# Performance work log

Measured on AMD Instinct MI355X. Metric: run time of the kernel, lower is better.

Reference implementation:

```python
import jax, jax.numpy as jnp
import numpy as np

N, E = 40000, 640000
IN_DIM, EDGE_DIM, HID, H1 = 5, 11, 128, 4
NEG_SLOPE = 0.2


def _add_self_loops(ei, ea, n):
    # PyG GATConv default: add_self_loops=True, fill_value='mean' for edge_attr
    loop = jnp.arange(n, dtype=ei.dtype)
    ei2 = jnp.concatenate([ei, jnp.stack([loop, loop])], axis=1)
    ea2 = jnp.concatenate([ea, jnp.broadcast_to(ea.mean(0), (n, ea.shape[1]))], axis=0)
    return ei2, ea2


def _gat(x, ei, ea, W, We, a_src, a_dst, a_edge, b, H, C):
    # Single GATConv layer (eval mode, dropout inactive)
    n = x.shape[0]
    xh = (x @ W).reshape(n, H, C)            # [N,H,C]
    eh = (ea @ We).reshape(-1, H, C)         # [E,H,C]
    src, dst = ei[0], ei[1]
    a_s = (xh * a_src).sum(-1)               # [N,H]
    a_d = (xh * a_dst).sum(-1)               # [N,H]
    alpha = jax.nn.leaky_relu(a_s[src] + a_d[dst] + (eh * a_edge).sum(-1), NEG_SLOPE)  # [E,H]
    amax = jax.ops.segment_max(alpha, dst, num_segments=n)
    ex = jnp.exp(alpha - amax[dst])
    den = jax.ops.segment_sum(ex, dst, num_segments=n)
    w = ex / (den[dst] + 1e-16)              # softmax over inbound edges per dst
    out = jax.ops.segment_sum(xh[src] * w[:, :, None], dst, num_segments=n)  # [N,H,C]
    return out.reshape(n, H * C) + b


def setup_inputs() -> dict:
    key = jax.random.key(0)
    ks = jax.random.split(key, 20)
    s = 0.1
    return {
        "x": jax.random.normal(ks[0], (N, IN_DIM), jnp.float32),
        "edge_index": jax.random.randint(ks[1], (2, E), 0, N),
        "edge_attr": jax.random.normal(ks[2], (E, EDGE_DIM), jnp.float32),
        "W1": jax.random.normal(ks[3], (IN_DIM, H1 * HID), jnp.float32) * s,
        "We1": jax.random.normal(ks[4], (EDGE_DIM, H1 * HID), jnp.float32) * s,
        "a_src1": jax.random.normal(ks[5], (H1, HID), jnp.float32) * s,
        "a_dst1": jax.random.normal(ks[6], (H1, HID), jnp.float32) * s,
        "a_edge1": jax.random.normal(ks[7], (H1, HID), jnp.float32) * s,
        "b1": jnp.zeros((H1 * HID,), jnp.float32),
        # layer 2 (512 -> 128, 1 head)
        "W2": jax.random.normal(ks[8], (H1 * HID, HID), jnp.float32) * s,
        "We2": jax.random.normal(ks[9], (EDGE_DIM, HID), jnp.float32) * s,
        "a_src2": jax.random.normal(ks[10], (1, HID), jnp.float32) * s,
        "a_dst2": jax.random.normal(ks[11], (1, HID), jnp.float32) * s,
        "a_edge2": jax.random.normal(ks[12], (1, HID), jnp.float32) * s,
        "b2": jnp.zeros((HID,), jnp.float32),
        # final linear 128 -> 1
        "Wfc": jax.random.normal(ks[13], (HID, 1), jnp.float32) * s,
        "bfc": jnp.zeros((1,), jnp.float32),
    }


def reference(x, edge_index, edge_attr,
              W1, We1, a_src1, a_dst1, a_edge1, b1,
              W2, We2, a_src2, a_dst2, a_edge2, b2,
              Wfc, bfc):
    ei, ea = _add_self_loops(edge_index, edge_attr, x.shape[0])
    h = jax.nn.relu(_gat(x, ei, ea, W1, We1, a_src1, a_dst1, a_edge1, b1, H1, HID))
    h = jax.nn.relu(_gat(h, ei, ea, W2, We2, a_src2, a_dst2, a_edge2, b2, 1, HID))
    return jax.nn.sigmoid(h @ Wfc + bfc)
```

## Files before the change

kernel.cpp:

```cpp
#include <hip/hip_runtime.h>

#define NN   40000
#define EE   640000
#define IND  5
#define ED   11
#define HIDD 128
#define F1   512
#define EB   1250

typedef unsigned short u16;
typedef unsigned int   u32;
typedef __attribute__((ext_vector_type(8))) short bf16x8;
typedef __attribute__((ext_vector_type(4))) float f32x4;

__device__ __forceinline__ float bf2f(u16 u) { return __uint_as_float(((u32)u) << 16); }
__device__ __forceinline__ u16 f2bf(float f) {
    u32 u = __float_as_uint(f);
    return (u16)((u + 0x7FFFu + ((u >> 16) & 1u)) >> 16);
}

__device__ __forceinline__ float wsum(float v) {
#pragma unroll
    for (int o = 32; o; o >>= 1) v += __shfl_xor(v, o, 64);
    return v;
}
__device__ __forceinline__ float lrelu(float v) { return v > 0.f ? v : 0.2f * v; }


#define SBLK 256
#define SGRID ((NN + SBLK - 1) / SBLK)
#define PREPG (EB + 33)

__global__ void __launch_bounds__(256) k_prep(const int* __restrict__ ei,
                                              int* __restrict__ counts,
                                              int* __restrict__ rank,
                                              float* __restrict__ consts,
                                              const float* __restrict__ ea,
                                              float* __restrict__ psum,
                                              const float* __restrict__ We1,
                                              const float* __restrict__ ae1,
                                              const float* __restrict__ We2,
                                              const float* __restrict__ ae2,
                                              const float* __restrict__ W2,
                                              u16* __restrict__ bsw,
                                              const float* __restrict__ W1,
                                              const float* __restrict__ as1,
                                              const float* __restrict__ ad1) {
    __shared__ float shf[4 * ED];
    int bid = blockIdx.x, t = threadIdx.x;
    if (bid < EB) {
        int i0 = bid * 512 + t;
        int i1 = i0 + 256;
        int d0 = ei[EE + i0];
        int d1 = ei[EE + i1];
        int rk0 = atomicAdd(&counts[d0], 1);
        int rk1 = atomicAdd(&counts[d1], 1);
        rank[i0] = rk0;
        rank[i1] = rk1;
        const float* r0 = ea + (size_t)i0 * ED;
        const float* r1 = ea + (size_t)i1 * ED;
        float r[ED];
#pragma unroll
        for (int k = 0; k < ED; ++k) r[k] = r0[k] + r1[k];
#pragma unroll
        for (int k = 0; k < ED; ++k) r[k] = wsum(r[k]);
        int wv = t >> 6, lane = t & 63;
#pragma unroll
        for (int k = 0; k < ED; ++k)
            if (lane == k) shf[wv * ED + k] = r[k];
        __syncthreads();
        if (t < ED)
            psum[(size_t)bid * ED + t] =
                shf[t] + shf[ED + t] + shf[2 * ED + t] + shf[3 * ED + t];
        return;
    }
    if (bid == EB) {
        if (t < 44) {
            int k = t >> 2, h = t & 3;
            float s = 0.f;
            for (int c = 0; c < HIDD; ++c)
                s += We1[k * F1 + h * HIDD + c] * ae1[h * HIDD + c];
            consts[16 + t] = s;
        }
        if (t >= 48 && t < 48 + ED) {
            int k = t - 48;
            float s = 0.f;
            for (int c = 0; c < HIDD; ++c)
                s += We2[k * HIDD + c] * ae2[c];
            consts[64 + k] = s;
        }
        if (t >= 64 && t < 84) {
            int idx = t - 64, j = idx >> 2, h = idx & 3;
            float s = 0.f;
            for (int c = 0; c < HIDD; ++c)
                s += W1[j * F1 + h * HIDD + c] * as1[h * HIDD + c];
            consts[100 + idx] = s;
        }
        if (t >= 84 && t < 104) {
            int idx = t - 84, j = idx >> 2, h = idx & 3;
            float s = 0.f;
            for (int c = 0; c < HIDD; ++c)
                s += W1[j * F1 + h * HIDD + c] * ad1[h * HIDD + c];
            consts[120 + idx] = s;
        }
        return;
    }
    int t2 = (bid - (EB + 1)) * 256 + t;
    if (t2 >= 8192) return;
    int lane = t2 & 63, ks = (t2 >> 6) & 15, nt = t2 >> 10;
    int kbase = ks * 32 + (lane >> 4) * 8;
    int n = nt * 16 + (lane & 15);
    size_t dst = (size_t)t2 * 8;
#pragma unroll
    for (int j = 0; j < 8; ++j)
        bsw[dst + j] = f2bf(W2[(size_t)(kbase + j) * HIDD + n]);
}

__global__ void __launch_bounds__(SBLK) k_scan(const int* __restrict__ counts,
                                               int* __restrict__ row_off,
                                               const float* __restrict__ x,
                                               float* __restrict__ consts,
                                               float* __restrict__ aS1,
                                               float* __restrict__ aD1,
                                               const float* __restrict__ psum) {
    __shared__ int shi[SBLK];
    __shared__ float shf[4 * ED];
    __shared__ float mean[ED];
    __shared__ int s_boff;
    int t = threadIdx.x, b = blockIdx.x;
    if (b < SGRID) {
        int acc = 0;
        for (int i = t; i < b * SBLK; i += SBLK) acc += counts[i];
        shi[t] = acc;
        __syncthreads();
        for (int o = 128; o; o >>= 1) {
            if (t < o) shi[t] += shi[t + o];
            __syncthreads();
        }
        if (t == 0) s_boff = shi[0];
        __syncthreads();
        int boff = s_boff;
        __syncthreads();
        int i = b * SBLK + t;
        int v = (i < NN) ? counts[i] : 0;
        shi[t] = v;
        __syncthreads();
        for (int o = 1; o < SBLK; o <<= 1) {
            int u = (t >= o) ? shi[t - o] : 0;
            __syncthreads();
            shi[t] += u;
            __syncthreads();
        }
        if (i < NN) row_off[i] = boff + shi[t] - v;
        if (b == 0 && t == 0) row_off[NN] = EE;
        return;
    }
    if (b == SGRID * 2) {
        float acc[ED];
#pragma unroll
        for (int k = 0; k < ED; ++k) acc[k] = 0.f;
        for (int w = t; w < EB; w += SBLK) {
            const float* p = psum + (size_t)w * ED;
#pragma unroll
            for (int k = 0; k < ED; ++k) acc[k] += p[k];
        }
#pragma unroll
        for (int k = 0; k < ED; ++k) acc[k] = wsum(acc[k]);
        int wv = t >> 6, lane = t & 63;
#pragma unroll
        for (int k = 0; k < ED; ++k)
            if (lane == k) shf[wv * ED + k] = acc[k];
        __syncthreads();
        if (t < ED)
            mean[t] = (shf[t] + shf[ED + t] + shf[2 * ED + t] + shf[3 * ED + t])
                      * (1.0f / (float)EE);
        __syncthreads();
        if (t < 4) {
            float s = 0.f;
            for (int k = 0; k < ED; ++k) s += mean[k] * consts[16 + k * 4 + t];
            consts[80 + t] = s;
        }
        if (t == 8) {
            float s = 0.f;
            for (int k = 0; k < ED; ++k) s += mean[k] * consts[64 + k];
            consts[96] = s;
        }
        return;
    }
    int n = (b - SGRID) * SBLK + t;
    if (n >= NN) return;
    const float* xp = x + (size_t)n * IND;
    float xv0 = xp[0], xv1 = xp[1], xv2 = xp[2], xv3 = xp[3], xv4 = xp[4];
    float4 s4, d4;
    float* sp = (float*)&s4;
    float* dp = (float*)&d4;
#pragma unroll
    for (int h = 0; h < 4; ++h) {
        sp[h] = xv0 * consts[100 + 0 * 4 + h] + xv1 * consts[100 + 1 * 4 + h]
              + xv2 * consts[100 + 2 * 4 + h] + xv3 * consts[100 + 3 * 4 + h]
              + xv4 * consts[100 + 4 * 4 + h];
        dp[h] = xv0 * consts[120 + 0 * 4 + h] + xv1 * consts[120 + 1 * 4 + h]
              + xv2 * consts[120 + 2 * 4 + h] + xv3 * consts[120 + 3 * 4 + h]
              + xv4 * consts[120 + 4 * 4 + h];
    }
    *(float4*)(aS1 + (size_t)n * 4) = s4;
    *(float4*)(aD1 + (size_t)n * 4) = d4;
}

__global__ void __launch_bounds__(256) k_build(const float* __restrict__ ea,
                                               const int* __restrict__ ei,
                                               const int* __restrict__ rank,
                                               const int* __restrict__ row_off,
                                               const float* __restrict__ consts,
                                               uint4* __restrict__ rec) {
    int t = threadIdx.x;
    int i0 = blockIdx.x * 512 + t;
    int i1 = i0 + 256;
    int s0v = ei[i0], s1v = ei[i1];
    int d0 = ei[EE + i0], d1 = ei[EE + i1];
    int p0 = row_off[d0] + rank[i0];
    int p1 = row_off[d1] + rank[i1];
    const float* r0 = ea + (size_t)i0 * ED;
    const float* r1 = ea + (size_t)i1 * ED;
    float a0 = 0.f, a1 = 0.f, a2 = 0.f, a3 = 0.f, a4 = 0.f;
    float b0 = 0.f, b1 = 0.f, b2 = 0.f, b3 = 0.f, b4 = 0.f;
#pragma unroll
    for (int k = 0; k < ED; ++k) {
        float c0 = consts[16 + k * 4 + 0], c1 = consts[16 + k * 4 + 1];
        float c2 = consts[16 + k * 4 + 2], c3 = consts[16 + k * 4 + 3];
        float ct = consts[64 + k];
        float v0 = r0[k], v1 = r1[k];
        a0 += v0 * c0; a1 += v0 * c1; a2 += v0 * c2; a3 += v0 * c3; a4 += v0 * ct;
        b0 += v1 * c0; b1 += v1 * c1; b2 += v1 * c2; b3 += v1 * c3; b4 += v1 * ct;
    }
    uint4 q0, q1;
    q0.x = (u32)f2bf(a0) | ((u32)f2bf(a1) << 16);
    q0.y = (u32)f2bf(a2) | ((u32)f2bf(a3) << 16);
    q0.z = (u32)s0v;
    q0.w = __float_as_uint(a4);
    q1.x = (u32)f2bf(b0) | ((u32)f2bf(b1) << 16);
    q1.y = (u32)f2bf(b2) | ((u32)f2bf(b3) << 16);
    q1.z = (u32)s1v;
    q1.w = __float_as_uint(b4);
    rec[p0] = q0;
    rec[p1] = q1;
}

__global__ void __launch_bounds__(256) k_agg1g(const int* __restrict__ row_off,
                                               const uint4* __restrict__ rec,
                                               const float* __restrict__ aS1,
                                               const float* __restrict__ aD1,
                                               const float* __restrict__ x,
                                               const float* __restrict__ W1,
                                               const float* __restrict__ b1,
                                               const float* __restrict__ consts,
                                               const u16* __restrict__ bsw,
                                               const float* __restrict__ as2,
                                               const float* __restrict__ ad2,
                                               u16* __restrict__ xh2,
                                               float* __restrict__ aS2,
                                               float* __restrict__ aD2) {
    __shared__ u16 hA[16 * 512];
    __shared__ float sh_ps[4][16], sh_pd[4][16];
    int wv = threadIdx.x >> 6, lane = threadIdx.x & 63;
    int g = lane >> 4, sl = lane & 15;
    int row = wv * 4 + g;
    int n0 = blockIdx.x * 16;
    int n = n0 + row;
    int s0 = row_off[n], s1 = row_off[n + 1];
    float4 adv = *(const float4*)(aD1 + (size_t)n * 4);
    float z0 = 0.f, z1 = 0.f, z2 = 0.f, z3 = 0.f;
    float xa[4][5];
#pragma unroll
    for (int h = 0; h < 4; ++h)
#pragma unroll
        for (int j = 0; j < 5; ++j) xa[h][j] = 0.f;

    for (int i = s0 + sl; i < s1; i += 16) {
        uint4 q = rec[i];
        int s = (int)q.z;
        float e0 = bf2f((u16)(q.x & 0xFFFF)), e1 = bf2f((u16)(q.x >> 16));
        float e2 = bf2f((u16)(q.y & 0xFFFF)), e3 = bf2f((u16)(q.y >> 16));
        float4 as4 = *(const float4*)(aS1 + (size_t)s * 4);
        const float* xp = x + (size_t)s * IND;
        float x0 = xp[0], x1 = xp[1], x2 = xp[2], x3 = xp[3], x4 = xp[4];
        float ex;
        ex = __expf(lrelu(e0 + as4.x + adv.x)); z0 += ex;
        xa[0][0] += ex * x0; xa[0][1] += ex * x1; xa[0][2] += ex * x2;
        xa[0][3] += ex * x3; xa[0][4] += ex * x4;
        ex = __expf(lrelu(e1 + as4.y + adv.y)); z1 += ex;
        xa[1][0] += ex * x0; xa[1][1] += ex * x1; xa[1][2] += ex * x2;
        xa[1][3] += ex * x3; xa[1][4] += ex * x4;
        ex = __expf(lrelu(e2 + as4.z + adv.z)); z2 += ex;
        xa[2][0] += ex * x0; xa[2][1] += ex * x1; xa[2][2] += ex * x2;
        xa[2][3] += ex * x3; xa[2][4] += ex * x4;
        ex = __expf(lrelu(e3 + as4.w + adv.w)); z3 += ex;
        xa[3][0] += ex * x0; xa[3][1] += ex * x1; xa[3][2] += ex * x2;
        xa[3][3] += ex * x3; xa[3][4] += ex * x4;
    }
    if (sl == 0) {
        float4 as4 = *(const float4*)(aS1 + (size_t)n * 4);
        const float* xp = x + (size_t)n * IND;
        float x0 = xp[0], x1 = xp[1], x2 = xp[2], x3 = xp[3], x4 = xp[4];
        float ex;
        ex = __expf(lrelu(consts[80] + as4.x + adv.x)); z0 += ex;
        xa[0][0] += ex * x0; xa[0][1] += ex * x1; xa[0][2] += ex * x2;
        xa[0][3] += ex * x3; xa[0][4] += ex * x4;
        ex = __expf(lrelu(consts[81] + as4.y + adv.y)); z1 += ex;
        xa[1][0] += ex * x0; xa[1][1] += ex * x1; xa[1][2] += ex * x2;
        xa[1][3] += ex * x3; xa[1][4] += ex * x4;
        ex = __expf(lrelu(consts[82] + as4.z + adv.z)); z2 += ex;
        xa[2][0] += ex * x0; xa[2][1] += ex * x1; xa[2][2] += ex * x2;
        xa[2][3] += ex * x3; xa[2][4] += ex * x4;
        ex = __expf(lrelu(consts[83] + as4.w + adv.w)); z3 += ex;
        xa[3][0] += ex * x0; xa[3][1] += ex * x1; xa[3][2] += ex * x2;
        xa[3][3] += ex * x3; xa[3][4] += ex * x4;
    }
#pragma unroll
    for (int o = 1; o <= 8; o <<= 1) {
        z0 += __shfl_xor(z0, o, 64); z1 += __shfl_xor(z1, o, 64);
        z2 += __shfl_xor(z2, o, 64); z3 += __shfl_xor(z3, o, 64);
#pragma unroll
        for (int h = 0; h < 4; ++h)
#pragma unroll
            for (int j = 0; j < 5; ++j) xa[h][j] += __shfl_xor(xa[h][j], o, 64);
    }
    float zz[4] = {z0, z1, z2, z3};
#pragma unroll
    for (int cb = 0; cb < 4; ++cb) {
        float ih = 1.f / (zz[cb] + 1e-16f);
        int c0 = cb * 128 + sl * 8;
        u32 wp[4];
#pragma unroll
        for (int jj = 0; jj < 4; ++jj) {
            int c = c0 + jj * 2;
            float v0 = (xa[cb][0] * W1[0 * F1 + c] + xa[cb][1] * W1[1 * F1 + c]
                      + xa[cb][2] * W1[2 * F1 + c] + xa[cb][3] * W1[3 * F1 + c]
                      + xa[cb][4] * W1[4 * F1 + c]) * ih;
            float v1 = (xa[cb][0] * W1[0 * F1 + c + 1] + xa[cb][1] * W1[1 * F1 + c + 1]
                      + xa[cb][2] * W1[2 * F1 + c + 1] + xa[cb][3] * W1[3 * F1 + c + 1]
                      + xa[cb][4] * W1[4 * F1 + c + 1]) * ih;
            v0 = fmaxf(v0 + b1[c], 0.f);
            v1 = fmaxf(v1 + b1[c + 1], 0.f);
            wp[jj] = (u32)f2bf(v0) | ((u32)f2bf(v1) << 16);
        }
        uint4 st; st.x = wp[0]; st.y = wp[1]; st.z = wp[2]; st.w = wp[3];
        int cbyte = (cb * 256 + sl * 16) ^ ((row & 7) << 4);
        *(uint4*)((char*)hA + row * 1024 + cbyte) = st;
    }
    __syncthreads();

    int mrow = lane & 15, quad = lane >> 4;
    const u16* bbase = bsw + lane * 8;
    int nt0 = wv * 2;
    f32x4 acc0 = (f32x4){0.f, 0.f, 0.f, 0.f};
    f32x4 acc1 = (f32x4){0.f, 0.f, 0.f, 0.f};
    const char* arow = (const char*)hA + mrow * 1024;
    int axor = (mrow & 7) << 4;
    bf16x8 af0 = *(const bf16x8*)(arow + ((quad * 16 + 0) ^ axor));
    bf16x8 af1;
    bf16x8 b00 = *(const bf16x8*)(bbase + (size_t)nt0 * 8192);
    bf16x8 b01 = *(const bf16x8*)(bbase + (size_t)(nt0 + 1) * 8192);
    bf16x8 n00, n01;
#pragma unroll
    for (int ks = 0; ks < 16; ++ks) {
        if (ks < 15) {
            af1 = *(const bf16x8*)(arow + ((quad * 16 + (ks + 1) * 64) ^ axor));
            n00 = *(const bf16x8*)(bbase + (size_t)nt0 * 8192 + (ks + 1) * 512);
            n01 = *(const bf16x8*)(bbase + (size_t)(nt0 + 1) * 8192 + (ks + 1) * 512);
        }
        acc0 = __builtin_amdgcn_mfma_f32_16x16x32_bf16(af0, b00, acc0, 0, 0, 0);
        acc1 = __builtin_amdgcn_mfma_f32_16x16x32_bf16(af0, b01, acc1, 0, 0, 0);
        af0 = af1; b00 = n00; b01 = n01;
    }
    float ps[4] = {0.f, 0.f, 0.f, 0.f}, pd[4] = {0.f, 0.f, 0.f, 0.f};
    {
        int col = nt0 * 16 + mrow;
        float sa = as2[col], da = ad2[col];
#pragma unroll
        for (int r = 0; r < 4; ++r) {
            float v = acc0[r];
            xh2[(size_t)(n0 + quad * 4 + r) * HIDD + col] = f2bf(v);
            ps[r] += v * sa; pd[r] += v * da;
        }
    }
    {
        int col = (nt0 + 1) * 16 + mrow;
        float sa = as2[col], da = ad2[col];
#pragma unroll
        for (int r = 0; r < 4; ++r) {
            float v = acc1[r];
            xh2[(size_t)(n0 + quad * 4 + r) * HIDD + col] = f2bf(v);
            ps[r] += v * sa; pd[r] += v * da;
        }
    }
#pragma unroll
    for (int r = 0; r < 4; ++r) {
#pragma unroll
        for (int o = 1; o <= 8; o <<= 1) {
            ps[r] += __shfl_xor(ps[r], o, 64);
            pd[r] += __shfl_xor(pd[r], o, 64);
        }
        if (mrow == 0) {
            sh_ps[wv][quad * 4 + r] = ps[r];
            sh_pd[wv][quad * 4 + r] = pd[r];
        }
    }
    __syncthreads();
    int t = threadIdx.x;
    if (t < 16) {
        float s = sh_ps[0][t] + sh_ps[1][t] + sh_ps[2][t] + sh_ps[3][t];
        aS2[n0 + t] = s;
    } else if (t < 32) {
        int r = t - 16;
        float s = sh_pd[0][r] + sh_pd[1][r] + sh_pd[2][r] + sh_pd[3][r];
        aD2[n0 + r] = s;
    }
}

__global__ void __launch_bounds__(256) k_agg2(const int* __restrict__ row_off,
                                              const uint4* __restrict__ rec,
                                              const float* __restrict__ aS2,
                                              const float* __restrict__ aD2,
                                              const u16* __restrict__ xh2,
                                              const float* __restrict__ bias2,
                                              const float* __restrict__ Wfc,
                                              const float* __restrict__ bfc,
                                              const float* __restrict__ consts,
                                              float* __restrict__ out) {
    int n = blockIdx.x * 4 + (threadIdx.x >> 6);
    int t = threadIdx.x & 63;
    int s0 = row_off[n], s1 = row_off[n + 1];
    float adn = aD2[n];
    int g = t >> 4, l = t & 15;
    int c0 = l * 8;
    float z = 0.f;
    float acc[8];
#pragma unroll
    for (int j = 0; j < 8; ++j) acc[j] = 0.f;
    for (int i = s0 + g; i < s1; i += 4) {
        uint4 qe = rec[i];
        int s = (int)qe.z;
        float et2 = __uint_as_float(qe.w);
        float ex = __expf(lrelu(aS2[s] + adn + et2));
        z += ex;
        uint4 q = *(const uint4*)(xh2 + (size_t)s * HIDD + c0);
        acc[0] += ex * bf2f((u16)(q.x & 0xFFFF)); acc[1] += ex * bf2f((u16)(q.x >> 16));
        acc[2] += ex * bf2f((u16)(q.y & 0xFFFF)); acc[3] += ex * bf2f((u16)(q.y >> 16));
        acc[4] += ex * bf2f((u16)(q.z & 0xFFFF)); acc[5] += ex * bf2f((u16)(q.z >> 16));
        acc[6] += ex * bf2f((u16)(q.w & 0xFFFF)); acc[7] += ex * bf2f((u16)(q.w >> 16));
    }
    if (g == 0) {
        float ex = __expf(lrelu(aS2[n] + adn + consts[96]));
        z += ex;
        uint4 q = *(const uint4*)(xh2 + (size_t)n * HIDD + c0);
        acc[0] += ex * bf2f((u16)(q.x & 0xFFFF)); acc[1] += ex * bf2f((u16)(q.x >> 16));
        acc[2] += ex * bf2f((u16)(q.y & 0xFFFF)); acc[3] += ex * bf2f((u16)(q.y >> 16));
        acc[4] += ex * bf2f((u16)(q.z & 0xFFFF)); acc[5] += ex * bf2f((u16)(q.z >> 16));
        acc[6] += ex * bf2f((u16)(q.w & 0xFFFF)); acc[7] += ex * bf2f((u16)(q.w >> 16));
    }
#pragma unroll
    for (int o = 16; o <= 32; o <<= 1) {
        z += __shfl_xor(z, o, 64);
#pragma unroll
        for (int j = 0; j < 8; ++j) acc[j] += __shfl_xor(acc[j], o, 64);
    }
    float inv = 1.f / (z + 1e-16f);
    float p = 0.f;
#pragma unroll
    for (int j = 0; j < 8; ++j) {
        float o = fmaxf(acc[j] * inv + bias2[c0 + j], 0.f);
        p += o * Wfc[c0 + j];
    }
#pragma unroll
    for (int o = 1; o <= 8; o <<= 1) p += __shfl_xor(p, o, 64);
    if (t == 0) {
        float logit = p + bfc[0];
        out[n] = 1.f / (1.f + __expf(-logit));
    }
}

extern "C" void kernel_launch(void* const* d_in, const int* in_sizes, int n_in,
                              void* d_out, int out_size, void* d_ws, size_t ws_size,
                              hipStream_t stream) {
    (void)in_sizes; (void)n_in; (void)out_size; (void)ws_size;
    const float* x   = (const float*)d_in[0];
    const int*   ei  = (const int*)d_in[1];
    const float* ea  = (const float*)d_in[2];
    const float* W1  = (const float*)d_in[3];
    const float* We1 = (const float*)d_in[4];
    const float* as1 = (const float*)d_in[5];
    const float* ad1 = (const float*)d_in[6];
    const float* ae1 = (const float*)d_in[7];
    const float* b1  = (const float*)d_in[8];
    const float* W2  = (const float*)d_in[9];
    const float* We2 = (const float*)d_in[10];
    const float* as2 = (const float*)d_in[11];
    const float* ad2 = (const float*)d_in[12];
    const float* ae2 = (const float*)d_in[13];
    const float* b2v = (const float*)d_in[14];
    const float* Wfc = (const float*)d_in[15];
    const float* bfc = (const float*)d_in[16];
    float* out = (float*)d_out;

    char* ws = (char*)d_ws;
    size_t off = 0;
    auto take = [&](size_t nb) {
        size_t r = off;
        off += (nb + 255) & ~(size_t)255;
        return r;
    };
    float* consts = (float*)(ws + take(1024));
    int*   counts = (int*)(ws + take((size_t)NN * 4));
    size_t zbytes = off;
    int* row_off  = (int*)(ws + take((size_t)(NN + 1) * 4));
    int* rank     = (int*)(ws + take((size_t)EE * 4));
    float* psum   = (float*)(ws + take((size_t)EB * ED * 4));
    uint4* rec    = (uint4*)(ws + take((size_t)EE * 16));
    float* aS1    = (float*)(ws + take((size_t)NN * 16));
    float* aD1    = (float*)(ws + take((size_t)NN * 16));
    float* aS2    = (float*)(ws + take((size_t)NN * 4));
    float* aD2    = (float*)(ws + take((size_t)NN * 4));
    u16* xh2      = (u16*)(ws + take((size_t)NN * HIDD * 2));
    u16* w2b      = (u16*)(ws + take((size_t)65536 * 2));

    hipMemsetAsync(ws, 0, zbytes, stream);
    k_prep<<<PREPG, 256, 0, stream>>>(ei, counts, rank, consts, ea, psum,
                                      We1, ae1, We2, ae2, W2, w2b, W1, as1, ad1);
    k_scan<<<SGRID * 2 + 1, SBLK, 0, stream>>>(counts, row_off, x, consts,
                                               aS1, aD1, psum);
    k_build<<<EB, 256, 0, stream>>>(ea, ei, rank, row_off, consts, rec);
    k_agg1g<<<2500, 256, 0, stream>>>(row_off, rec, aS1, aD1, x, W1, b1, consts,
                                      w2b, as2, ad2, xh2, aS2, aD2);
    k_agg2<<<NN / 4, 256, 0, stream>>>(row_off, rec, aS2, aD2, xh2, b2v, Wfc, bfc,
                                       consts, out);
}
```

Baseline: 234.5 us.

## Double agg1 block tile to 32 nodes so each wave reuses one B tile

The fused layer-1 aggregation plus layer-2 projection kernel now processes 32 destination nodes per 512-thread block instead of 16 per 256-thread block. In the MFMA phase each of 8 waves owns a single 16-column slice of W2 and applies it to two 16-row A tiles, so B fragments are loaded once and reused twice. Before, each wave loaded two B tiles for one A tile. This halves global reads of the swizzled W2 per node. The cost is doubled LDS per block and fewer, larger blocks, which may reduce occupancy and tail balance.

```diff
diff --git a/kernel.cpp b/kernel.cpp
--- a/kernel.cpp
+++ b/kernel.cpp
@@ -7,6 +7,7 @@
 #define HIDD 128
 #define F1   512
 #define EB   1250
+#define AGB  1250
 
 typedef unsigned short u16;
 typedef unsigned int   u32;
@@ -246,7 +247,7 @@
     rec[p1] = q1;
 }
 
-__global__ void __launch_bounds__(256) k_agg1g(const int* __restrict__ row_off,
+__global__ void __launch_bounds__(512) k_agg1g(const int* __restrict__ row_off,
                                                const uint4* __restrict__ rec,
                                                const float* __restrict__ aS1,
                                                const float* __restrict__ aD1,
@@ -260,12 +261,12 @@
                                                u16* __restrict__ xh2,
                                                float* __restrict__ aS2,
                                                float* __restrict__ aD2) {
-    __shared__ u16 hA[16 * 512];
-    __shared__ float sh_ps[4][16], sh_pd[4][16];
+    __shared__ u16 hA[32 * 512];
+    __shared__ float sh_ps[2][8][16], sh_pd[2][8][16];
     int wv = threadIdx.x >> 6, lane = threadIdx.x & 63;
     int g = lane >> 4, sl = lane & 15;
     int row = wv * 4 + g;
-    int n0 = blockIdx.x * 16;
+    int n0 = blockIdx.x * 32;
     int n = n0 + row;
     int s0 = row_off[n], s1 = row_off[n + 1];
     float4 adv = *(const float4*)(aD1 + (size_t)n * 4);
@@ -351,70 +352,66 @@
     __syncthreads();
 
     int mrow = lane & 15, quad = lane >> 4;
-    const u16* bbase = bsw + lane * 8;
-    int nt0 = wv * 2;
-    f32x4 acc0 = (f32x4){0.f, 0.f, 0.f, 0.f};
-    f32x4 acc1 = (f32x4){0.f, 0.f, 0.f, 0.f};
-    const char* arow = (const char*)hA + mrow * 1024;
+    const u16* bbase = bsw + lane * 8 + (size_t)wv * 8192;
+    f32x4 accA = (f32x4){0.f, 0.f, 0.f, 0.f};
+    f32x4 accB = (f32x4){0.f, 0.f, 0.f, 0.f};
+    const char* arowA = (const char*)hA + mrow * 1024;
+    const char* arowB = (const char*)hA + (16 + mrow) * 1024;
     int axor = (mrow & 7) << 4;
-    bf16x8 af0 = *(const bf16x8*)(arow + ((quad * 16 + 0) ^ axor));
-    bf16x8 af1;
-    bf16x8 b00 = *(const bf16x8*)(bbase + (size_t)nt0 * 8192);
-    bf16x8 b01 = *(const bf16x8*)(bbase + (size_t)(nt0 + 1) * 8192);
-    bf16x8 n00, n01;
+    bf16x8 afA0 = *(const bf16x8*)(arowA + ((quad * 16 + 0) ^ axor));
+    bf16x8 afB0 = *(const bf16x8*)(arowB + ((quad * 16 + 0) ^ axor));
+    bf16x8 afA1, afB1;
+    bf16x8 b0 = *(const bf16x8*)(bbase);
+    bf16x8 bn;
 #pragma unroll
     for (int ks = 0; ks < 16; ++ks) {
         if (ks < 15) {
-            af1 = *(const bf16x8*)(arow + ((quad * 16 + (ks + 1) * 64) ^ axor));
-            n00 = *(const bf16x8*)(bbase + (size_t)nt0 * 8192 + (ks + 1) * 512);
-            n01 = *(const bf16x8*)(bbase + (size_t)(nt0 + 1) * 8192 + (ks + 1) * 512);
-        }
-        acc0 = __builtin_amdgcn_mfma_f32_16x16x32_bf16(af0, b00, acc0, 0, 0, 0);
-        acc1 = __builtin_amdgcn_mfma_f32_16x16x32_bf16(af0, b01, acc1, 0, 0, 0);
-        af0 = af1; b00 = n00; b01 = n01;
-    }
-    float ps[4] = {0.f, 0.f, 0.f, 0.f}, pd[4] = {0.f, 0.f, 0.f, 0.f};
-    {
-        int col = nt0 * 16 + mrow;
-        float sa = as2[col], da = ad2[col];
-#pragma unroll
-        for (int r = 0; r < 4; ++r) {
-            float v = acc0[r];
-            xh2[(size_t)(n0 + quad * 4 + r) * HIDD + col] = f2bf(v);
-            ps[r] += v * sa; pd[r] += v * da;
-        }
-    }
-    {
-        int col = (nt0 + 1) * 16 + mrow;
-        float sa = as2[col], da = ad2[col];
-#pragma unroll
-        for (int r = 0; r < 4; ++r) {
-            float v = acc1[r];
-            xh2[(size_t)(n0 + quad * 4 + r) * HIDD + col] = f2bf(v);
-            ps[r] += v * sa; pd[r] += v * da;
-        }
-    }
+            afA1 = *(const bf16x8*)(arowA + ((quad * 16 + (ks + 1) * 64) ^ axor));
+            afB1 = *(const bf16x8*)(arowB + ((quad * 16 + (ks + 1) * 64) ^ axor));
+            bn = *(const bf16x8*)(bbase + (ks + 1) * 512);
+        }
+        accA = __builtin_amdgcn_mfma_f32_16x16x32_bf16(afA0, b0, accA, 0, 0, 0);
+        accB = __builtin_amdgcn_mfma_f32_16x16x32_bf16(afB0, b0, accB, 0, 0, 0);
+        afA0 = afA1; afB0 = afB1; b0 = bn;
+    }
+    int col = wv * 16 + mrow;
+    float sa = as2[col], da = ad2[col];
+    float psA[4], pdA[4], psB[4], pdB[4];
 #pragma unroll
     for (int r = 0; r < 4; ++r) {
+        float vA = accA[r];
+        xh2[(size_t)(n0 + quad * 4 + r) * HIDD + col] = f2bf(vA);
+        psA[r] = vA * sa; pdA[r] = vA * da;
+        float vB = accB[r];
+        xh2[(size_t)(n0 + 16 + quad * 4 + r) * HIDD + col] = f2bf(vB);
+        psB[r] = vB * sa; pdB[r] = vB * da;
+    }
+#pragma unroll
+    for (int r = 0; r < 4; ++r) {
 #pragma unroll
         for (int o = 1; o <= 8; o <<= 1) {
-            ps[r] += __shfl_xor(ps[r], o, 64);
-            pd[r] += __shfl_xor(pd[r], o, 64);
+            psA[r] += __shfl_xor(psA[r], o, 64);
+            pdA[r] += __shfl_xor(pdA[r], o, 64);
+            psB[r] += __shfl_xor(psB[r], o, 64);
+            pdB[r] += __shfl_xor(pdB[r], o, 64);
         }
         if (mrow == 0) {
-            sh_ps[wv][quad * 4 + r] = ps[r];
-            sh_pd[wv][quad * 4 + r] = pd[r];
+            sh_ps[0][wv][quad * 4 + r] = psA[r];
+            sh_pd[0][wv][quad * 4 + r] = pdA[r];
+            sh_ps[1][wv][quad * 4 + r] = psB[r];
+            sh_pd[1][wv][quad * 4 + r] = pdB[r];
         }
     }
     __syncthreads();
     int t = threadIdx.x;
-    if (t < 16) {
-        float s = sh_ps[0][t] + sh_ps[1][t] + sh_ps[2][t] + sh_ps[3][t];
-        aS2[n0 + t] = s;
-    } else if (t < 32) {
-        int r = t - 16;
-        float s = sh_pd[0][r] + sh_pd[1][r] + sh_pd[2][r] + sh_pd[3][r];
-        aD2[n0 + r] = s;
+    if (t < 64) {
+        int tile = t >> 5, isD = (t >> 4) & 1, r = t & 15;
+        float s = 0.f;
+#pragma unroll
+        for (int w = 0; w < 8; ++w)
+            s += isD ? sh_pd[tile][w][r] : sh_ps[tile][w][r];
+        int node = n0 + tile * 16 + r;
+        if (isD) aD2[node] = s; else aS2[node] = s;
     }
 }
 
@@ -530,8 +527,8 @@
     k_scan<<<SGRID * 2 + 1, SBLK, 0, stream>>>(counts, row_off, x, consts,
                                                aS1, aD1, psum);
     k_build<<<EB, 256, 0, stream>>>(ea, ei, rank, row_off, consts, rec);
-    k_agg1g<<<2500, 256, 0, stream>>>(row_off, rec, aS1, aD1, x, W1, b1, consts,
-                                      w2b, as2, ad2, xh2, aS2, aD2);
+    k_agg1g<<<AGB, 512, 0, stream>>>(row_off, rec, aS1, aD1, x, W1, b1, consts,
+                                     w2b, as2, ad2, xh2, aS2, aD2);
     k_agg2<<<NN / 4, 256, 0, stream>>>(row_off, rec, aS2, aD2, xh2, b2v, Wfc, bfc,
                                        consts, out);
 }
```

Result: no change. 238.1 us (+1.6%).
